# Kernel optimization log

Measured on AMD Instinct MI355X. Metric: run time of the kernel, lower is better.

## Reference

```python
import jax, jax.numpy as jnp
import numpy as np

UNITS = 2048

def _cat_complex(Wr, Wi):
    # real-matrix representation of complex matmul: [[Wr, -Wi], [Wi, Wr]]
    top = jnp.concatenate([Wr, -Wi], axis=-1)
    bot = jnp.concatenate([Wi, Wr], axis=-1)
    return jnp.concatenate([top, bot], axis=0)

def _hard_sigmoid(x):
    return jnp.clip(0.2 * x + 0.5, 0.0, 1.0)

def setup_inputs() -> dict:
    key = jax.random.key(0)
    ks = jax.random.split(key, 8)
    B, IN2, U3 = 1024, 4096, 3 * UNITS
    s_in = 1.0 / np.sqrt(IN2)
    s_h = 1.0 / np.sqrt(2 * UNITS)
    return {
        "inputs": jax.random.normal(ks[0], (B, IN2), jnp.float32),
        "h_tm1": jax.random.normal(ks[1], (B, 2 * UNITS), jnp.float32),
        "real_kernel": jax.random.normal(ks[2], (IN2 // 2, U3), jnp.float32) * s_in,
        "imaginary_kernel": jax.random.normal(ks[3], (IN2 // 2, U3), jnp.float32) * s_in,
        "real_recurrent_kernel": jax.random.normal(ks[4], (UNITS, U3), jnp.float32) * s_h,
        "imaginary_recurrent_kernel": jax.random.normal(ks[5], (UNITS, U3), jnp.float32) * s_h,
        "real_bias": jax.random.normal(ks[6], (U3,), jnp.float32) * 0.01,
        "imaginary_bias": jax.random.normal(ks[7], (U3,), jnp.float32) * 0.01,
    }

def reference(inputs, h_tm1, real_kernel, imaginary_kernel,
              real_recurrent_kernel, imaginary_recurrent_kernel,
              real_bias, imaginary_bias):
    u = UNITS
    # per-gate complex kernels in real [[Wr,-Wi],[Wi,Wr]] form
    Kz = _cat_complex(real_kernel[:, :u], imaginary_kernel[:, :u])
    Kr = _cat_complex(real_kernel[:, u:2 * u], imaginary_kernel[:, u:2 * u])
    Kh = _cat_complex(real_kernel[:, 2 * u:], imaginary_kernel[:, 2 * u:])
    Rz = _cat_complex(real_recurrent_kernel[:, :u], imaginary_recurrent_kernel[:, :u])
    Rr = _cat_complex(real_recurrent_kernel[:, u:2 * u], imaginary_recurrent_kernel[:, u:2 * u])
    Rh = _cat_complex(real_recurrent_kernel[:, 2 * u:], imaginary_recurrent_kernel[:, 2 * u:])
    bz = jnp.concatenate([real_bias[:u], imaginary_bias[:u]])
    br = jnp.concatenate([real_bias[u:2 * u], imaginary_bias[u:2 * u]])
    bh = jnp.concatenate([real_bias[2 * u:], imaginary_bias[2 * u:]])
    # implementation=1, reset_after=False, no dropout
    x_z = inputs @ Kz + bz
    x_r = inputs @ Kr + br
    x_h = inputs @ Kh + bh
    z = _hard_sigmoid(x_z + h_tm1 @ Rz)
    r = _hard_sigmoid(x_r + h_tm1 @ Rr)
    hh = jnp.tanh(x_h + (r * h_tm1) @ Rh)
    h = z * h_tm1 + (1.0 - z) * hh
    return h
```

## Files before the change

kernel.cpp:

```cpp
#include <hip/hip_runtime.h>

typedef _Float16 half8  __attribute__((ext_vector_type(8)));
typedef _Float16 half4v __attribute__((ext_vector_type(4)));
typedef _Float16 half2v __attribute__((ext_vector_type(2)));
typedef float    float4v __attribute__((ext_vector_type(4)));

__device__ __forceinline__ float hsig(float x) {
  return fminf(fmaxf(fmaf(x, 0.2f, 0.5f), 0.0f), 1.0f);
}

__global__ __launch_bounds__(256) void cvt_pair(const float* __restrict__ src,
                                                _Float16* __restrict__ d1,
                                                _Float16* __restrict__ d2) {
  int i = blockIdx.x * blockDim.x + threadIdx.x;
  int base = i * 4;
  int j = base & 4095;
  float s = (j < 2048) ? -1.0f : 1.0f;
  float4 v = *(const float4*)&src[base];
  half4v h1 = {(_Float16)v.x, (_Float16)v.y, (_Float16)v.z, (_Float16)v.w};
  half4v h2 = {(_Float16)(s * v.x), (_Float16)(s * v.y), (_Float16)(s * v.z), (_Float16)(s * v.w)};
  *(half4v*)&d1[base] = h1;
  *(half4v*)&d2[base] = h2;
}

__global__ __launch_bounds__(256) void transpose_cast(
    const float* __restrict__ s0, const float* __restrict__ s1,
    const float* __restrict__ s2, const float* __restrict__ s3,
    _Float16* __restrict__ d0, _Float16* __restrict__ d1m,
    _Float16* __restrict__ d2m, _Float16* __restrict__ d3m)
{
  __shared__ float tile[64][65];
  const float* srcs[4] = {s0, s1, s2, s3};
  _Float16*    dsts[4] = {d0, d1m, d2m, d3m};
  const float* src = srcs[blockIdx.z];
  _Float16*    dst = dsts[blockIdx.z];

  const int tid = threadIdx.x;
  const int k0 = blockIdx.x * 64;
  const int j0 = blockIdx.y * 64;

  const int tx = tid & 63, ty = tid >> 6;
#pragma unroll
  for (int r = 0; r < 64; r += 4)
    tile[r + ty][tx] = src[(size_t)(k0 + r + ty) * 6144 + j0 + tx];
  __syncthreads();

  const int txk = (tid & 31) * 2;
  const int tyn = tid >> 5;
#pragma unroll
  for (int r = 0; r < 64; r += 8) {
    int jl = r + tyn;
    half2v p = {(_Float16)tile[txk][jl], (_Float16)tile[txk + 1][jl]};
    *(half2v*)&dst[(size_t)(j0 + jl) * 2048 + k0 + txk] = p;
  }
}

__global__ __launch_bounds__(256) void rgate(const _Float16* __restrict__ xacc,
                                             const float* __restrict__ h,
                                             _Float16* __restrict__ A1r,
                                             _Float16* __restrict__ A2r) {
  int i = blockIdx.x * blockDim.x + threadIdx.x;
  int base = i * 4;
  int m = base >> 12;
  int j = base & 4095;
  float s = (j < 2048) ? -1.0f : 1.0f;
  half4v rp = *(const half4v*)&xacc[(size_t)m * 12288 + 4096 + j];
  float4 hv = *(const float4*)&h[base];
  float p0 = hsig((float)rp[0]) * hv.x;
  float p1 = hsig((float)rp[1]) * hv.y;
  float p2 = hsig((float)rp[2]) * hv.z;
  float p3 = hsig((float)rp[3]) * hv.w;
  half4v o1 = {(_Float16)p0, (_Float16)p1, (_Float16)p2, (_Float16)p3};
  half4v o2 = {(_Float16)(s * p0), (_Float16)(s * p1), (_Float16)(s * p2), (_Float16)(s * p3)};
  *(half4v*)&A1r[base] = o1;
  *(half4v*)&A2r[base] = o2;
}

template<int FINAL>
__global__ __launch_bounds__(256) void gemm_big(
    const _Float16* __restrict__ Ax1, const _Float16* __restrict__ Ax2,
    const _Float16* __restrict__ Ah1, const _Float16* __restrict__ Ah2,
    const _Float16* __restrict__ WKr, const _Float16* __restrict__ WKi,
    const _Float16* __restrict__ WRr, const _Float16* __restrict__ WRi,
    _Float16* __restrict__ xacc, float* __restrict__ out,
    const float* __restrict__ h_tm1,
    const float* __restrict__ rbias, const float* __restrict__ ibias)
{
  __shared__ __align__(16) _Float16 lds[32768];
  const int tid  = threadIdx.x;
  const int lane = tid & 63;
  const int wave = tid >> 6;
  const int quad = lane >> 4;
  const int r16  = lane & 15;
  const int wm = (wave >> 1) * 64;
  const int wn = (wave & 1) * 64;
  const int mbase = blockIdx.y * 128;
  const int nbase = blockIdx.x * 128;

  const int  gate   = nbase >> 12;
  const bool hi     = (nbase & 2048) != 0;
  const int  jprime = nbase & 2047;
  const size_t browK = (size_t)(gate * 2048 + jprime) * 2048;

  int nph;
  const _Float16* pA[4];
  const _Float16* pB[4];
  if (FINAL) {
    nph = 2;
    const _Float16* Ax = hi ? Ax2 : Ax1;
    const _Float16* BL = hi ? WKi : WKr;
    const _Float16* BH = hi ? WKr : WKi;
    pA[0] = Ax + (size_t)mbase * 4096;      pB[0] = BL + (size_t)jprime * 2048;
    pA[1] = pA[0] + 2048;                   pB[1] = BH + (size_t)jprime * 2048;
  } else {
    const _Float16* Ax = hi ? Ax2 : Ax1;
    const _Float16* KL = hi ? WKi : WKr;
    const _Float16* KH = hi ? WKr : WKi;
    pA[0] = Ax + (size_t)mbase * 4096;      pB[0] = KL + browK;
    pA[1] = pA[0] + 2048;                   pB[1] = KH + browK;
    if (gate < 2) {
      nph = 4;
      const _Float16* Ah = hi ? Ah2 : Ah1;
      const _Float16* RL = hi ? WRi : WRr;
      const _Float16* RH = hi ? WRr : WRi;
      pA[2] = Ah + (size_t)mbase * 4096;    pB[2] = RL + browK;
      pA[3] = pA[2] + 2048;                 pB[3] = RH + browK;
    } else {
      nph = 2;
    }
  }

  float4v acc[4][4];
#pragma unroll
  for (int i = 0; i < 4; ++i)
#pragma unroll
    for (int j = 0; j < 4; ++j) acc[i][j] = (float4v){0.f, 0.f, 0.f, 0.f};

  int offA[8], offB[8], ldsA[8], ldsB[8];
#pragma unroll
  for (int i = 0; i < 8; ++i) {
    int c = i * 256 + tid;
    int row = c >> 4;
    int sw = (c & 15) ^ (row & 7);
    offA[i] = row * 4096 + sw * 8;
    offB[i] = row * 2048 + sw * 8;
    ldsA[i] = c * 8;
    ldsB[i] = 16384 + c * 8;
  }

  for (int p = 0; p < nph; ++p) {
    const _Float16* Ab = pA[p];
    const _Float16* Bb = pB[p];
    for (int it = 0; it < 16; ++it) {
#pragma unroll
      for (int i = 0; i < 8; ++i)
        __builtin_amdgcn_global_load_lds(
            (__attribute__((address_space(1))) void*)(Ab + offA[i]),
            (__attribute__((address_space(3))) void*)&lds[ldsA[i]], 16, 0, 0);
#pragma unroll
      for (int i = 0; i < 8; ++i)
        __builtin_amdgcn_global_load_lds(
            (__attribute__((address_space(1))) void*)(Bb + offB[i]),
            (__attribute__((address_space(3))) void*)&lds[ldsB[i]], 16, 0, 0);
      Ab += 128;
      Bb += 128;
      __syncthreads();
#pragma unroll
      for (int ks = 0; ks < 4; ++ks) {
        half8 af[4], bf[4];
        int akg = ks * 4 + quad;
#pragma unroll
        for (int t = 0; t < 4; ++t) {
          int arow = wm + t * 16 + r16;
          af[t] = *(const half8*)&lds[(arow * 16 + (akg ^ (arow & 7))) * 8];
          int brow = wn + t * 16 + r16;
          bf[t] = *(const half8*)&lds[16384 + (brow * 16 + (akg ^ (brow & 7))) * 8];
        }
#pragma unroll
        for (int mt = 0; mt < 4; ++mt)
#pragma unroll
          for (int nt = 0; nt < 4; ++nt)
            acc[mt][nt] = __builtin_amdgcn_mfma_f32_16x16x32_f16(af[mt], bf[nt], acc[mt][nt], 0, 0, 0);
      }
      __syncthreads();
    }
  }

  const int mrow0 = mbase + wm + quad * 4;
  const int ncol0 = nbase + wn + r16;
  if (!FINAL) {
#pragma unroll
    for (int nt = 0; nt < 4; ++nt) {
      int n = ncol0 + nt * 16;
      int g = n >> 12, j = n & 4095;
      float b = (j < 2048) ? rbias[g * 2048 + j] : ibias[g * 2048 + j - 2048];
#pragma unroll
      for (int mt = 0; mt < 4; ++mt)
#pragma unroll
        for (int e = 0; e < 4; ++e) {
          int m = mrow0 + mt * 16 + e;
          xacc[(size_t)m * 12288 + n] = (_Float16)(acc[mt][nt][e] + b);
        }
    }
  } else {
#pragma unroll
    for (int nt = 0; nt < 4; ++nt) {
      int n = ncol0 + nt * 16;
#pragma unroll
      for (int mt = 0; mt < 4; ++mt)
#pragma unroll
        for (int e = 0; e < 4; ++e) {
          int m = mrow0 + mt * 16 + e;
          float z  = hsig((float)xacc[(size_t)m * 12288 + n]);
          float xh = (float)xacc[(size_t)m * 12288 + 8192 + n];
          float hh = tanhf(xh + acc[mt][nt][e]);
          float ht = h_tm1[(size_t)m * 4096 + n];
          out[(size_t)m * 4096 + n] = z * ht + (1.0f - z) * hh;
        }
    }
  }
}

extern "C" void kernel_launch(void* const* d_in, const int* in_sizes, int n_in,
                              void* d_out, int out_size, void* d_ws, size_t ws_size,
                              hipStream_t stream) {
  const float* inputs = (const float*)d_in[0];
  const float* h_tm1  = (const float*)d_in[1];
  const float* rk     = (const float*)d_in[2];
  const float* ik     = (const float*)d_in[3];
  const float* rrk    = (const float*)d_in[4];
  const float* irk    = (const float*)d_in[5];
  const float* rb     = (const float*)d_in[6];
  const float* ib     = (const float*)d_in[7];
  float* out = (float*)d_out;

  char* ws = (char*)d_ws;
  _Float16* WrK  = (_Float16*)(ws + 0);
  _Float16* WiK  = (_Float16*)(ws + 25165824);
  _Float16* WrR  = (_Float16*)(ws + 50331648);
  _Float16* WiR  = (_Float16*)(ws + 75497472);
  _Float16* A1x  = (_Float16*)(ws + 100663296);
  _Float16* A2x  = (_Float16*)(ws + 109051904);
  _Float16* A1h  = (_Float16*)(ws + 117440512);
  _Float16* A2h  = (_Float16*)(ws + 125829120);
  _Float16* xacc = (_Float16*)(ws + 134217728);
  _Float16* A1r  = A1x;
  _Float16* A2r  = A2x;

  cvt_pair<<<4096, 256, 0, stream>>>(inputs, A1x, A2x);
  cvt_pair<<<4096, 256, 0, stream>>>(h_tm1, A1h, A2h);
  transpose_cast<<<dim3(32, 96, 4), 256, 0, stream>>>(rk, ik, rrk, irk, WrK, WiK, WrR, WiR);
  gemm_big<0><<<dim3(96, 8), 256, 0, stream>>>(A1x, A2x, A1h, A2h, WrK, WiK, WrR, WiR,
                                               xacc, nullptr, nullptr, rb, ib);
  rgate<<<4096, 256, 0, stream>>>(xacc, h_tm1, A1r, A2r);
  gemm_big<1><<<dim3(32, 8), 256, 0, stream>>>(A1r, A2r, nullptr, nullptr,
                                               WrR + (size_t)4096 * 2048,
                                               WiR + (size_t)4096 * 2048,
                                               nullptr, nullptr, xacc, out, h_tm1,
                                               nullptr, nullptr);
}
```

Before: 605.1 us.

## Split-K the final GEMM, halve the LDS tile, and add a combine kernel

The final candidate-state GEMM is split along K into two halves over a z grid dimension, which doubles its block count from 256. Each half writes fp16 partial sums to scratch buffers, and a new elementwise kernel adds them and applies the gate epilogue. The shared K tile is cut from 128 to 64, halving LDS per block, and launch bounds now request 3 blocks per CU so occupancy can rise. The cost is an extra launch, a round trip of the partials through memory, rounding partials to fp16, and more barriers per K step.

```diff
diff --git a/kernel.cpp b/kernel.cpp
--- a/kernel.cpp
+++ b/kernel.cpp
@@ -76,17 +76,51 @@
   *(half4v*)&A2r[base] = o2;
 }
 
+__global__ __launch_bounds__(256) void combine(const _Float16* __restrict__ xacc,
+                                               const _Float16* __restrict__ P0,
+                                               const _Float16* __restrict__ P1,
+                                               const float* __restrict__ h,
+                                               float* __restrict__ out) {
+  int i = blockIdx.x * blockDim.x + threadIdx.x;
+  int base = i * 4;
+  int m = base >> 12;
+  int j = base & 4095;
+  half4v zv = *(const half4v*)&xacc[(size_t)m * 12288 + j];
+  half4v xh = *(const half4v*)&xacc[(size_t)m * 12288 + 8192 + j];
+  half4v p0 = *(const half4v*)&P0[base];
+  half4v p1 = *(const half4v*)&P1[base];
+  float4 hv = *(const float4*)&h[base];
+  float4 o;
+  {
+    float z = hsig((float)zv[0]); float t = tanhf((float)xh[0] + (float)p0[0] + (float)p1[0]);
+    o.x = z * hv.x + (1.0f - z) * t;
+  }
+  {
+    float z = hsig((float)zv[1]); float t = tanhf((float)xh[1] + (float)p0[1] + (float)p1[1]);
+    o.y = z * hv.y + (1.0f - z) * t;
+  }
+  {
+    float z = hsig((float)zv[2]); float t = tanhf((float)xh[2] + (float)p0[2] + (float)p1[2]);
+    o.z = z * hv.z + (1.0f - z) * t;
+  }
+  {
+    float z = hsig((float)zv[3]); float t = tanhf((float)xh[3] + (float)p0[3] + (float)p1[3]);
+    o.w = z * hv.w + (1.0f - z) * t;
+  }
+  *(float4*)&out[base] = o;
+}
+
 template<int FINAL>
-__global__ __launch_bounds__(256) void gemm_big(
+__global__ __launch_bounds__(256, 3) void gemm_big(
     const _Float16* __restrict__ Ax1, const _Float16* __restrict__ Ax2,
     const _Float16* __restrict__ Ah1, const _Float16* __restrict__ Ah2,
     const _Float16* __restrict__ WKr, const _Float16* __restrict__ WKi,
     const _Float16* __restrict__ WRr, const _Float16* __restrict__ WRi,
-    _Float16* __restrict__ xacc, float* __restrict__ out,
-    const float* __restrict__ h_tm1,
+    _Float16* __restrict__ xacc,
+    _Float16* __restrict__ P0, _Float16* __restrict__ P1,
     const float* __restrict__ rbias, const float* __restrict__ ibias)
 {
-  __shared__ __align__(16) _Float16 lds[32768];
+  __shared__ __align__(16) _Float16 lds[16384];
   const int tid  = threadIdx.x;
   const int lane = tid & 63;
   const int wave = tid >> 6;
@@ -100,19 +134,24 @@
   const int  gate   = nbase >> 12;
   const bool hi     = (nbase & 2048) != 0;
   const int  jprime = nbase & 2047;
-  const size_t browK = (size_t)(gate * 2048 + jprime) * 2048;
 
   int nph;
   const _Float16* pA[4];
   const _Float16* pB[4];
   if (FINAL) {
-    nph = 2;
+    nph = 1;
     const _Float16* Ax = hi ? Ax2 : Ax1;
     const _Float16* BL = hi ? WKi : WKr;
     const _Float16* BH = hi ? WKr : WKi;
-    pA[0] = Ax + (size_t)mbase * 4096;      pB[0] = BL + (size_t)jprime * 2048;
-    pA[1] = pA[0] + 2048;                   pB[1] = BH + (size_t)jprime * 2048;
+    if (blockIdx.z == 0) {
+      pA[0] = Ax + (size_t)mbase * 4096;
+      pB[0] = BL + (size_t)jprime * 2048;
+    } else {
+      pA[0] = Ax + (size_t)mbase * 4096 + 2048;
+      pB[0] = BH + (size_t)jprime * 2048;
+    }
   } else {
+    const size_t browK = (size_t)(gate * 2048 + jprime) * 2048;
     const _Float16* Ax = hi ? Ax2 : Ax1;
     const _Float16* KL = hi ? WKi : WKr;
     const _Float16* KH = hi ? WKr : WKi;
@@ -136,45 +175,48 @@
 #pragma unroll
     for (int j = 0; j < 4; ++j) acc[i][j] = (float4v){0.f, 0.f, 0.f, 0.f};
 
-  int offA[8], offB[8], ldsA[8], ldsB[8];
-#pragma unroll
-  for (int i = 0; i < 8; ++i) {
+  int offA[4], offB[4], ldsA[4], ldsB[4];
+#pragma unroll
+  for (int i = 0; i < 4; ++i) {
     int c = i * 256 + tid;
-    int row = c >> 4;
-    int sw = (c & 15) ^ (row & 7);
+    int row = c >> 3;
+    int sw = (c & 7) ^ (row & 7);
     offA[i] = row * 4096 + sw * 8;
     offB[i] = row * 2048 + sw * 8;
     ldsA[i] = c * 8;
-    ldsB[i] = 16384 + c * 8;
-  }
-
-  for (int p = 0; p < nph; ++p) {
+    ldsB[i] = 8192 + c * 8;
+  }
+
+#pragma unroll 1
+  for (int p = 0; p < 4; ++p) {
+    if (p >= nph) break;
     const _Float16* Ab = pA[p];
     const _Float16* Bb = pB[p];
-    for (int it = 0; it < 16; ++it) {
-#pragma unroll
-      for (int i = 0; i < 8; ++i)
+#pragma unroll 1
+    for (int it = 0; it < 32; ++it) {
+#pragma unroll
+      for (int i = 0; i < 4; ++i)
         __builtin_amdgcn_global_load_lds(
             (__attribute__((address_space(1))) void*)(Ab + offA[i]),
             (__attribute__((address_space(3))) void*)&lds[ldsA[i]], 16, 0, 0);
 #pragma unroll
-      for (int i = 0; i < 8; ++i)
+      for (int i = 0; i < 4; ++i)
         __builtin_amdgcn_global_load_lds(
             (__attribute__((address_space(1))) void*)(Bb + offB[i]),
             (__attribute__((address_space(3))) void*)&lds[ldsB[i]], 16, 0, 0);
-      Ab += 128;
-      Bb += 128;
+      Ab += 64;
+      Bb += 64;
       __syncthreads();
 #pragma unroll
-      for (int ks = 0; ks < 4; ++ks) {
+      for (int ks = 0; ks < 2; ++ks) {
         half8 af[4], bf[4];
         int akg = ks * 4 + quad;
 #pragma unroll
         for (int t = 0; t < 4; ++t) {
           int arow = wm + t * 16 + r16;
-          af[t] = *(const half8*)&lds[(arow * 16 + (akg ^ (arow & 7))) * 8];
+          af[t] = *(const half8*)&lds[(arow * 8 + (akg ^ (arow & 7))) * 8];
           int brow = wn + t * 16 + r16;
-          bf[t] = *(const half8*)&lds[16384 + (brow * 16 + (akg ^ (brow & 7))) * 8];
+          bf[t] = *(const half8*)&lds[8192 + (brow * 8 + (akg ^ (brow & 7))) * 8];
         }
 #pragma unroll
         for (int mt = 0; mt < 4; ++mt)
@@ -203,6 +245,7 @@
         }
     }
   } else {
+    _Float16* P = blockIdx.z ? P1 : P0;
 #pragma unroll
     for (int nt = 0; nt < 4; ++nt) {
       int n = ncol0 + nt * 16;
@@ -211,11 +254,7 @@
 #pragma unroll
         for (int e = 0; e < 4; ++e) {
           int m = mrow0 + mt * 16 + e;
-          float z  = hsig((float)xacc[(size_t)m * 12288 + n]);
-          float xh = (float)xacc[(size_t)m * 12288 + 8192 + n];
-          float hh = tanhf(xh + acc[mt][nt][e]);
-          float ht = h_tm1[(size_t)m * 4096 + n];
-          out[(size_t)m * 4096 + n] = z * ht + (1.0f - z) * hh;
+          P[(size_t)m * 4096 + n] = (_Float16)acc[mt][nt][e];
         }
     }
   }
@@ -246,6 +285,8 @@
   _Float16* xacc = (_Float16*)(ws + 134217728);
   _Float16* A1r  = A1x;
   _Float16* A2r  = A2x;
+  _Float16* P0   = A1h;
+  _Float16* P1   = A2h;
 
   cvt_pair<<<4096, 256, 0, stream>>>(inputs, A1x, A2x);
   cvt_pair<<<4096, 256, 0, stream>>>(h_tm1, A1h, A2h);
@@ -253,9 +294,10 @@
   gemm_big<0><<<dim3(96, 8), 256, 0, stream>>>(A1x, A2x, A1h, A2h, WrK, WiK, WrR, WiR,
                                                xacc, nullptr, nullptr, rb, ib);
   rgate<<<4096, 256, 0, stream>>>(xacc, h_tm1, A1r, A2r);
-  gemm_big<1><<<dim3(32, 8), 256, 0, stream>>>(A1r, A2r, nullptr, nullptr,
-                                               WrR + (size_t)4096 * 2048,
-                                               WiR + (size_t)4096 * 2048,
-                                               nullptr, nullptr, xacc, out, h_tm1,
-                                               nullptr, nullptr);
-}
+  gemm_big<1><<<dim3(32, 8, 2), 256, 0, stream>>>(A1r, A2r, nullptr, nullptr,
+                                                  WrR + (size_t)4096 * 2048,
+                                                  WiR + (size_t)4096 * 2048,
+                                                  nullptr, nullptr, nullptr, P0, P1,
+                                                  nullptr, nullptr);
+  combine<<<4096, 256, 0, stream>>>(xacc, P0, P1, h_tm1, out);
+}
```

Result: faster. 504.5 us (-16.6%).
